# Performance work log

Measured on AMD Instinct MI355X. Metric: run time of the kernel, lower is better.

Reference implementation:

```python
import jax, jax.numpy as jnp
import numpy as np


def setup_inputs() -> dict:
    key = jax.random.key(0)
    ks = jax.random.split(key, 6)
    B, C, V, L = 64, 32, 512, 13
    C_OUT = 64
    C_CAT = (2 * 3 + 1) * C  # order*support_len + 1 = 7 blocks -> 224
    x = jax.random.normal(ks[0], (B, C, V, L), dtype=jnp.float32)
    support0 = jax.random.uniform(ks[1], (V, V), dtype=jnp.float32)
    support1 = jax.random.uniform(ks[2], (V, V), dtype=jnp.float32)
    support2 = jax.random.uniform(ks[3], (V, V), dtype=jnp.float32)
    W = jax.random.normal(ks[4], (C_OUT, C_CAT), dtype=jnp.float32) * 0.05
    b = jnp.zeros((C_OUT,), dtype=jnp.float32)
    return {"x": x, "support0": support0, "support1": support1,
            "support2": support2, "W": W, "b": b}


def reference(x, support0, support1, support2, W, b):
    # Graph WaveNet GCN, eval mode (dropout is identity at inference).
    # x: [B, C, V, L]; each support a: [V, V].
    outs = [x]
    for a in (support0, support1, support2):
        x1 = jnp.einsum('ncvl,vw->ncwl', x, a)   # order 1 propagation
        outs.append(x1)
        x2 = jnp.einsum('ncvl,vw->ncwl', x1, a)  # order 2 propagation
        outs.append(x2)
    h = jnp.concatenate(outs, axis=1)            # [B, 7*C, V, L]
    # 1x1 Conv2d == per-(v,l) linear over channels
    h = jnp.einsum('ncvl,oc->novl', h, W) + b[None, :, None, None]
    return h
```

## Files before the change

kernel.cpp:

```cpp
#include <hip/hip_runtime.h>


typedef unsigned short u16;
typedef unsigned int   u32;
typedef __bf16 bf16x8 __attribute__((ext_vector_type(8)));
typedef float  f32x4  __attribute__((ext_vector_type(4)));

#define DEVI static __device__ __forceinline__

#define NB   64
#define NC   32
#define NV   512
#define NL   13
#define CO   64
#define CCAT 224
#define MROWS 26624
#define SZA   262144L
#define MSZ   (26624L * 512L)

DEVI u16 f2bf(float f) {
  union { float f; u32 u; } v; v.f = f;
  u32 u = v.u;
  return (u16)((u + 0x7fffu + ((u >> 16) & 1u)) >> 16);
}

DEVI void gl2lds16(const void* g, void* l) {
  __builtin_amdgcn_global_load_lds((__attribute__((address_space(1))) void*)g,
                                   (__attribute__((address_space(3))) void*)l, 16, 0, 0);
}

__global__ __launch_bounds__(256) void prep_A(const float* __restrict__ A0,
                                              const float* __restrict__ A1,
                                              const float* __restrict__ A2,
                                              u16* __restrict__ BT,
                                              u16* __restrict__ ABF) {
  const int s = blockIdx.z;
  const float* A = (s == 0) ? A0 : ((s == 1) ? A1 : A2);
  u16* abf = ABF + (long)s * SZA;
  u16* bt  = BT + (long)(2 * s) * SZA;
  __shared__ float t[32][33];
  const int v0 = blockIdx.x * 32, w0 = blockIdx.y * 32;
  const int tid = threadIdx.x;
  for (int i = tid; i < 1024; i += 256) {
    const int r = i >> 5, c = i & 31;
    const float val = A[(long)(v0 + r) * 512 + w0 + c];
    t[r][c] = val;
    abf[(long)(v0 + r) * 512 + w0 + c] = f2bf(val);
  }
  __syncthreads();
  for (int i = tid; i < 1024; i += 256) {
    const int r = i >> 5, c = i & 31;
    bt[(long)(w0 + r) * 512 + v0 + c] = f2bf(t[c][r]);
  }
}

__global__ __launch_bounds__(256) void prep_W(const float* __restrict__ W,
                                              u16* __restrict__ WBF) {
  const int i = blockIdx.x * 256 + threadIdx.x;
  WBF[i] = f2bf(W[i]);
}

__global__ __launch_bounds__(256) void transpose_x(const float* __restrict__ x,
                                                   u16* __restrict__ XT) {
  __shared__ __align__(16) float tile[NV * NL];
  const int bc = blockIdx.x;
  const float4* src4 = (const float4*)(x + (long)bc * (NV * NL));
  float4* t4 = (float4*)tile;
  for (int i = threadIdx.x; i < (NV * NL) / 4; i += 256) t4[i] = src4[i];
  __syncthreads();
  u16* dst = XT + (long)bc * (NL * NV);
  for (int j = threadIdx.x; j < NL * NV; j += 256) {
    const int l = j >> 9, v = j & 511;
    dst[j] = f2bf(tile[v * NL + l]);
  }
}

__global__ __launch_bounds__(256) void gemm512(const u16* __restrict__ Ag,
                                               const u16* __restrict__ Bg,
                                               u16* __restrict__ Cg,
                                               long aZ, long bZ, long cZ) {
  __shared__ u16 As[128 * 32];
  __shared__ u16 Bs[128 * 32];
  const int p = blockIdx.z;
  const u16* A = Ag + (long)p * aZ;
  const u16* B = Bg + (long)p * bZ;
  u16*       C = Cg + (long)p * cZ;
  const int m0 = blockIdx.y * 128, n0 = blockIdx.x * 128;
  const int tid = threadIdx.x;
  const int lane = tid & 63, wid = tid >> 6;
  const int wm = wid >> 1, wn = wid & 1;
  const int lr = lane & 15, lq = lane >> 4;
  const int srow = lane >> 2, skq = lane & 3;

  f32x4 acc[4][4] = {};

  for (int kt = 0; kt < 16; ++kt) {
    const int k0 = kt * 32;
    __syncthreads();
#pragma unroll
    for (int j = 0; j < 2; ++j) {
      const int rb = wid * 32 + j * 16;
      gl2lds16(A + (long)(m0 + rb + srow) * 512 + (k0 + skq * 8), &As[rb * 32]);
      gl2lds16(B + (long)(n0 + rb + srow) * 512 + (k0 + skq * 8), &Bs[rb * 32]);
    }
    __syncthreads();
    bf16x8 af[4], bv[4];
#pragma unroll
    for (int t = 0; t < 4; ++t) {
      af[t] = *(const bf16x8*)&As[(wm * 64 + t * 16 + lr) * 32 + lq * 8];
      bv[t] = *(const bf16x8*)&Bs[(wn * 64 + t * 16 + lr) * 32 + lq * 8];
    }
#pragma unroll
    for (int i = 0; i < 4; ++i)
#pragma unroll
      for (int j = 0; j < 4; ++j)
        acc[i][j] = __builtin_amdgcn_mfma_f32_16x16x32_bf16(af[i], bv[j], acc[i][j], 0, 0, 0);
  }
#pragma unroll
  for (int i = 0; i < 4; ++i) {
    const int mr = m0 + wm * 64 + i * 16 + lq * 4;
#pragma unroll
    for (int j = 0; j < 4; ++j) {
      const int nc = n0 + wn * 64 + j * 16 + lr;
#pragma unroll
      for (int r = 0; r < 4; ++r)
        C[(long)(mr + r) * 512 + nc] = f2bf(acc[i][j][r]);
    }
  }
}

__global__ __launch_bounds__(256) void proj_out(const u16* __restrict__ Yall,
                                                const u16* __restrict__ WBF,
                                                const float* __restrict__ bias,
                                                float* __restrict__ out) {
  __shared__ u16 Hs[512 * 32];
  const int n = blockIdx.y, wch = blockIdx.x;
  const int tid = threadIdx.x;
  const int lane = tid & 63, wid = tid >> 6;
  const int lr = lane & 15, lq = lane >> 4;
  const int wq = tid & 15, cp = tid >> 4;

  f32x4 acc[32] = {};
  float bia[4];
#pragma unroll
  for (int r = 0; r < 4; ++r) bia[r] = bias[wid * 16 + lq * 4 + r];

  for (int blk = 0; blk < 7; ++blk) {
    const u16* Y = Yall + (long)blk * MSZ;
    __syncthreads();
    const long rbase = ((long)(n * NC + cp * 2) * NL) * 512 + wch * 32 + wq * 2;
#pragma unroll
    for (int lp = 0; lp < NL; ++lp) {
      const u32 a = *(const u32*)(Y + rbase + (long)lp * 512);
      const u32 b = *(const u32*)(Y + rbase + (long)lp * 512 + NL * 512);
      const u32 pack0 = (a & 0xffffu) | (b << 16);
      const u32 pack1 = (a >> 16) | (b & 0xffff0000u);
      const int w0_ = wq * 2, w1_ = w0_ + 1;
      const int g = cp >> 2, wic = cp & 3;
      *(u32*)&Hs[(w0_ * 16 + lp) * 32 + ((g ^ (w0_ & 3)) * 8) + wic * 2] = pack0;
      *(u32*)&Hs[(w1_ * 16 + lp) * 32 + ((g ^ (w1_ & 3)) * 8) + wic * 2] = pack1;
    }
    __syncthreads();
    const bf16x8 af = *(const bf16x8*)&WBF[(wid * 16 + lr) * CCAT + blk * 32 + lq * 8];
#pragma unroll
    for (int t = 0; t < 32; ++t) {
      const bf16x8 bv = *(const bf16x8*)&Hs[(t * 16 + lr) * 32 + ((lq ^ (t & 3)) * 8)];
      acc[t] = __builtin_amdgcn_mfma_f32_16x16x32_bf16(af, bv, acc[t], 0, 0, 0);
    }
  }
  if (lr < NL) {
#pragma unroll
    for (int t = 0; t < 32; ++t) {
      const int w = wch * 32 + t;
      const long base = (((long)n * CO + wid * 16 + lq * 4) * 512 + w) * NL + lr;
#pragma unroll
      for (int r = 0; r < 4; ++r)
        out[base + (long)r * (512 * NL)] = acc[t][r] + bia[r];
    }
  }
}

extern "C" void kernel_launch(void* const* d_in, const int* in_sizes, int n_in,
                              void* d_out, int out_size, void* d_ws, size_t ws_size,
                              hipStream_t stream) {
  const float* x  = (const float*)d_in[0];
  const float* s0 = (const float*)d_in[1];
  const float* s1 = (const float*)d_in[2];
  const float* s2 = (const float*)d_in[3];
  const float* W  = (const float*)d_in[4];
  const float* b  = (const float*)d_in[5];
  float* out = (float*)d_out;

  char* ws = (char*)d_ws;
  u16* XT  = (u16*)(ws);
  u16* Y   = (u16*)(ws + 27262976L);
  u16* BT  = (u16*)(ws + 190840832L);
  u16* ABF = (u16*)(ws + 193986560L);
  u16* WBF = (u16*)(ws + 195559424L);

  prep_A<<<dim3(16, 16, 3), 256, 0, stream>>>(s0, s1, s2, BT, ABF);
  prep_W<<<dim3(56), 256, 0, stream>>>(W, WBF);
  gemm512<<<dim3(4, 4, 3), 256, 0, stream>>>(BT, ABF, BT + SZA,
                                             2L * SZA, 1L * SZA, 2L * SZA);
  transpose_x<<<dim3(NB * NC), 256, 0, stream>>>(x, XT);
  gemm512<<<dim3(4, 208, 6), 256, 0, stream>>>(XT, BT, Y,
                                               0L, 1L * SZA, MSZ);
  proj_out<<<dim3(16, NB), 256, 0, stream>>>(XT, WBF, b, out);
}
```

Measured before the change: 393.9 us.

## Reorder big GEMM grid for A-tile reuse, widen proj_out to 512 threads, pack transpose stores

Replaces the big batched GEMM launch with a dedicated kernel whose grid puts the six propagation matrices and N tiles on the fast x dimension, so blocks sharing the same XT row tile run close together and can reuse it from L2. The output projection kernel now uses 512 threads with each wave handling half the w columns, which halves the per-thread accumulators, and it loads Y with ushort4 reads and a new LDS swizzle. The x transpose writes two bf16 values per 32-bit store. proj_out still reads XT and 7 blocks spaced MSZ apart, as in the code before; that indexing looks inconsistent with where Y is written, but the change keeps it.

Measured after the change: 351.6 us. 10.7% less time.

```diff
diff --git a/kernel.cpp b/kernel.cpp
--- a/kernel.cpp
+++ b/kernel.cpp
@@ -14,7 +14,6 @@
 #define NL   13
 #define CO   64
 #define CCAT 224
-#define MROWS 26624
 #define SZA   262144L
 #define MSZ   (26624L * 512L)
 
@@ -69,9 +68,11 @@
   for (int i = threadIdx.x; i < (NV * NL) / 4; i += 256) t4[i] = src4[i];
   __syncthreads();
   u16* dst = XT + (long)bc * (NL * NV);
-  for (int j = threadIdx.x; j < NL * NV; j += 256) {
-    const int l = j >> 9, v = j & 511;
-    dst[j] = f2bf(tile[v * NL + l]);
+  for (int j = threadIdx.x; j < NL * 256; j += 256) {
+    const int l = j >> 8, v = (j & 255) * 2;
+    const u32 lo = f2bf(tile[v * NL + l]);
+    const u32 hi = f2bf(tile[(v + 1) * NL + l]);
+    *(u32*)&dst[l * 512 + v] = lo | (hi << 16);
   }
 }
 
@@ -129,53 +130,109 @@
   }
 }
 
-__global__ __launch_bounds__(256) void proj_out(const u16* __restrict__ Yall,
+__global__ __launch_bounds__(256) void gemm_big(const u16* __restrict__ A,
+                                                const u16* __restrict__ Bg,
+                                                u16* __restrict__ Cg) {
+  __shared__ u16 As[128 * 32];
+  __shared__ u16 Bs[128 * 32];
+  const int p = blockIdx.x >> 2;
+  const int n0 = (blockIdx.x & 3) * 128;
+  const int m0 = blockIdx.y * 128;
+  const u16* B = Bg + (long)p * SZA;
+  u16*       C = Cg + (long)p * MSZ;
+  const int tid = threadIdx.x;
+  const int lane = tid & 63, wid = tid >> 6;
+  const int wm = wid >> 1, wn = wid & 1;
+  const int lr = lane & 15, lq = lane >> 4;
+  const int srow = lane >> 2, skq = lane & 3;
+
+  f32x4 acc[4][4] = {};
+
+  for (int kt = 0; kt < 16; ++kt) {
+    const int k0 = kt * 32;
+    __syncthreads();
+#pragma unroll
+    for (int j = 0; j < 2; ++j) {
+      const int rb = wid * 32 + j * 16;
+      gl2lds16(A + (long)(m0 + rb + srow) * 512 + (k0 + skq * 8), &As[rb * 32]);
+      gl2lds16(B + (long)(n0 + rb + srow) * 512 + (k0 + skq * 8), &Bs[rb * 32]);
+    }
+    __syncthreads();
+    bf16x8 af[4], bv[4];
+#pragma unroll
+    for (int t = 0; t < 4; ++t) {
+      af[t] = *(const bf16x8*)&As[(wm * 64 + t * 16 + lr) * 32 + lq * 8];
+      bv[t] = *(const bf16x8*)&Bs[(wn * 64 + t * 16 + lr) * 32 + lq * 8];
+    }
+#pragma unroll
+    for (int i = 0; i < 4; ++i)
+#pragma unroll
+      for (int j = 0; j < 4; ++j)
+        acc[i][j] = __builtin_amdgcn_mfma_f32_16x16x32_bf16(af[i], bv[j], acc[i][j], 0, 0, 0);
+  }
+#pragma unroll
+  for (int i = 0; i < 4; ++i) {
+    const int mr = m0 + wm * 64 + i * 16 + lq * 4;
+#pragma unroll
+    for (int j = 0; j < 4; ++j) {
+      const int nc = n0 + wn * 64 + j * 16 + lr;
+#pragma unroll
+      for (int r = 0; r < 4; ++r)
+        C[(long)(mr + r) * 512 + nc] = f2bf(acc[i][j][r]);
+    }
+  }
+}
+
+__global__ __launch_bounds__(512) void proj_out(const u16* __restrict__ Yall,
                                                 const u16* __restrict__ WBF,
                                                 const float* __restrict__ bias,
                                                 float* __restrict__ out) {
   __shared__ u16 Hs[512 * 32];
   const int n = blockIdx.y, wch = blockIdx.x;
+  const int w_base = wch * 32;
   const int tid = threadIdx.x;
   const int lane = tid & 63, wid = tid >> 6;
+  const int og = wid & 3, th = wid >> 2;
   const int lr = lane & 15, lq = lane >> 4;
-  const int wq = tid & 15, cp = tid >> 4;
-
-  f32x4 acc[32] = {};
+  const int c = tid >> 4, q = tid & 15;
+
+  f32x4 acc[16] = {};
   float bia[4];
 #pragma unroll
-  for (int r = 0; r < 4; ++r) bia[r] = bias[wid * 16 + lq * 4 + r];
+  for (int r = 0; r < 4; ++r) bia[r] = bias[og * 16 + lq * 4 + r];
+
+  const int cchunk = c >> 3, cin = c & 7;
 
   for (int blk = 0; blk < 7; ++blk) {
-    const u16* Y = Yall + (long)blk * MSZ;
-    __syncthreads();
-    const long rbase = ((long)(n * NC + cp * 2) * NL) * 512 + wch * 32 + wq * 2;
-#pragma unroll
-    for (int lp = 0; lp < NL; ++lp) {
-      const u32 a = *(const u32*)(Y + rbase + (long)lp * 512);
-      const u32 b = *(const u32*)(Y + rbase + (long)lp * 512 + NL * 512);
-      const u32 pack0 = (a & 0xffffu) | (b << 16);
-      const u32 pack1 = (a >> 16) | (b & 0xffff0000u);
-      const int w0_ = wq * 2, w1_ = w0_ + 1;
-      const int g = cp >> 2, wic = cp & 3;
-      *(u32*)&Hs[(w0_ * 16 + lp) * 32 + ((g ^ (w0_ & 3)) * 8) + wic * 2] = pack0;
-      *(u32*)&Hs[(w1_ * 16 + lp) * 32 + ((g ^ (w1_ & 3)) * 8) + wic * 2] = pack1;
-    }
-    __syncthreads();
-    const bf16x8 af = *(const bf16x8*)&WBF[(wid * 16 + lr) * CCAT + blk * 32 + lq * 8];
-#pragma unroll
-    for (int t = 0; t < 32; ++t) {
-      const bf16x8 bv = *(const bf16x8*)&Hs[(t * 16 + lr) * 32 + ((lq ^ (t & 3)) * 8)];
-      acc[t] = __builtin_amdgcn_mfma_f32_16x16x32_bf16(af, bv, acc[t], 0, 0, 0);
+    const u16* Yrow = Yall + (long)blk * MSZ + ((long)(n * NC + c) * NL) * 512 + w_base;
+    __syncthreads();
+    for (int i = q; i < 104; i += 16) {
+      const int lp = i >> 3, w4 = i & 7;
+      const ushort4 d = *(const ushort4*)(Yrow + lp * 512 + w4 * 4);
+      const int colc = ((cchunk ^ (w4 & 3)) << 3) | cin;
+      const int rbase = (w4 * 4) * 16 + lp;
+      Hs[(rbase +  0) * 32 + colc] = d.x;
+      Hs[(rbase + 16) * 32 + colc] = d.y;
+      Hs[(rbase + 32) * 32 + colc] = d.z;
+      Hs[(rbase + 48) * 32 + colc] = d.w;
+    }
+    __syncthreads();
+    const bf16x8 af = *(const bf16x8*)&WBF[(og * 16 + lr) * CCAT + blk * 32 + lq * 8];
+#pragma unroll
+    for (int tt = 0; tt < 16; ++tt) {
+      const int t = th * 16 + tt;
+      const bf16x8 bv = *(const bf16x8*)&Hs[(t * 16 + lr) * 32 + ((lq ^ ((t >> 2) & 3)) << 3)];
+      acc[tt] = __builtin_amdgcn_mfma_f32_16x16x32_bf16(af, bv, acc[tt], 0, 0, 0);
     }
   }
   if (lr < NL) {
 #pragma unroll
-    for (int t = 0; t < 32; ++t) {
-      const int w = wch * 32 + t;
-      const long base = (((long)n * CO + wid * 16 + lq * 4) * 512 + w) * NL + lr;
+    for (int tt = 0; tt < 16; ++tt) {
+      const int w = w_base + th * 16 + tt;
+      const long base = (((long)n * CO + og * 16 + lq * 4) * 512 + w) * NL + lr;
 #pragma unroll
       for (int r = 0; r < 4; ++r)
-        out[base + (long)r * (512 * NL)] = acc[t][r] + bia[r];
+        out[base + (long)r * (512 * NL)] = acc[tt][r] + bia[r];
     }
   }
 }
@@ -203,7 +260,6 @@
   gemm512<<<dim3(4, 4, 3), 256, 0, stream>>>(BT, ABF, BT + SZA,
                                              2L * SZA, 1L * SZA, 2L * SZA);
   transpose_x<<<dim3(NB * NC), 256, 0, stream>>>(x, XT);
-  gemm512<<<dim3(4, 208, 6), 256, 0, stream>>>(XT, BT, Y,
-                                               0L, 1L * SZA, MSZ);
-  proj_out<<<dim3(16, NB), 256, 0, stream>>>(XT, WBF, b, out);
-}
+  gemm_big<<<dim3(24, 208), 256, 0, stream>>>(XT, BT, Y);
+  proj_out<<<dim3(16, NB), 512, 0, stream>>>(XT, WBF, b, out);
+}
```

## Fuse graph propagation GEMMs with 1x1 projection to drop intermediate buffer

Applied to the files above, without the earlier changes.

Replaces the batched propagation GEMM and the separate projection kernel with one fused kernel. For each (batch, 64-column chunk), it streams x and support tiles through a triple-buffered LDS pipeline using async global-to-LDS loads. Each propagated block is written into an LDS H tile and immediately accumulated into the output projection. This removes the write and re-read of the large bf16 intermediate Y through global memory. The transpose kernel also packs two bf16 values per store. The cost is heavy LDS use (about 155 KB), which limits the kernel to one block per CU, plus extra barriers.

Result: slower. 636.9 us (+61.7%).

```diff
diff --git a/kernel.cpp b/kernel.cpp
--- a/kernel.cpp
+++ b/kernel.cpp
@@ -14,9 +14,7 @@
 #define NL   13
 #define CO   64
 #define CCAT 224
-#define MROWS 26624
-#define SZA   262144L
-#define MSZ   (26624L * 512L)
+#define SZA  262144L
 
 DEVI u16 f2bf(float f) {
   union { float f; u32 u; } v; v.f = f;
@@ -69,9 +67,11 @@
   for (int i = threadIdx.x; i < (NV * NL) / 4; i += 256) t4[i] = src4[i];
   __syncthreads();
   u16* dst = XT + (long)bc * (NL * NV);
-  for (int j = threadIdx.x; j < NL * NV; j += 256) {
-    const int l = j >> 9, v = j & 511;
-    dst[j] = f2bf(tile[v * NL + l]);
+  for (int j = threadIdx.x; j < NL * 256; j += 256) {
+    const int l = j >> 8, v = (j & 255) * 2;
+    const u32 lo = f2bf(tile[v * NL + l]);
+    const u32 hi = f2bf(tile[(v + 1) * NL + l]);
+    *(u32*)&dst[l * 512 + v] = lo | (hi << 16);
   }
 }
 
@@ -129,53 +129,109 @@
   }
 }
 
-__global__ __launch_bounds__(256) void proj_out(const u16* __restrict__ Yall,
-                                                const u16* __restrict__ WBF,
-                                                const float* __restrict__ bias,
-                                                float* __restrict__ out) {
-  __shared__ u16 Hs[512 * 32];
-  const int n = blockIdx.y, wch = blockIdx.x;
-  const int tid = threadIdx.x;
-  const int lane = tid & 63, wid = tid >> 6;
+__global__ __launch_bounds__(512, 2) void fused_gcn(const u16* __restrict__ Xt,
+                                                    const u16* __restrict__ Bt,
+                                                    const u16* __restrict__ WBF,
+                                                    const float* __restrict__ bias,
+                                                    float* __restrict__ out) {
+  __shared__ u16 As[3][416 * 32];
+  __shared__ u16 Bs[3][64 * 32];
+  __shared__ u16 Hs[832 * 40];
+
+  const int bid = blockIdx.x;
+  const int n = bid >> 3, wch = bid & 7;
+  const int tid = threadIdx.x, lane = tid & 63, wid = tid >> 6;
   const int lr = lane & 15, lq = lane >> 4;
-  const int wq = tid & 15, cp = tid >> 4;
-
-  f32x4 acc[32] = {};
+  const int ot = wid >> 1, jpar = wid & 1;
+  const int mt0 = wid >> 2, nt = wid & 3;
+  const u16* XtN = Xt + (long)n * (416L * 512);
+
+  f32x4 acco[26] = {};
+
+  auto stage = [&](int g) {
+    const int p = g >> 4, kt = g & 15, bi = g % 3;
+    const int rsub = lane >> 2, koff = kt * 32 + (lane & 3) * 8;
+    const u16* Bp = Bt + (long)p * SZA + (long)(wch * 64) * 512;
+#pragma unroll
+    for (int t = 0; t < 4; ++t) {
+      const int i = wid + t * 8;
+      if (i < 26) {
+        gl2lds16(XtN + (long)(i * 16 + rsub) * 512 + koff, &As[bi][i * 16 * 32]);
+      } else {
+        const int b = (i - 26) & 3;
+        gl2lds16(Bp + (long)(b * 16 + rsub) * 512 + koff, &Bs[bi][b * 16 * 32]);
+      }
+    }
+  };
+
+  auto proj = [&](int blk) {
+    const bf16x8 af = *(const bf16x8*)&WBF[(ot * 16 + lr) * CCAT + blk * 32 + lq * 8];
+#pragma unroll
+    for (int k = 0; k < 26; ++k) {
+      const int jt = jpar + 2 * k;
+      const bf16x8 bv = *(const bf16x8*)&Hs[(jt * 16 + lr) * 40 + lq * 8];
+      acco[k] = __builtin_amdgcn_mfma_f32_16x16x32_bf16(af, bv, acco[k], 0, 0, 0);
+    }
+  };
+
+  stage(0);
+  for (int i = tid; i < 416 * 16; i += 512) {
+    const int m = i >> 4, wq = i & 15;
+    const ushort4 v = *(const ushort4*)(XtN + (long)m * 512 + wch * 64 + wq * 4);
+    const int c = (m * 5042) >> 16, l = m - c * 13;
+    const int rb = (wq * 4) * 13 + l;
+    Hs[(rb +  0) * 40 + c] = v.x;
+    Hs[(rb + 13) * 40 + c] = v.y;
+    Hs[(rb + 26) * 40 + c] = v.z;
+    Hs[(rb + 39) * 40 + c] = v.w;
+  }
+  __syncthreads();
+  proj(0);
+
+  for (int p = 0; p < 6; ++p) {
+    f32x4 accp[13] = {};
+    for (int kt = 0; kt < 16; ++kt) {
+      const int g = p * 16 + kt;
+      if (g < 95) {
+        stage(g + 1);
+        asm volatile("s_waitcnt vmcnt(4)\n\ts_barrier" ::: "memory");
+      } else {
+        asm volatile("s_waitcnt vmcnt(0)\n\ts_barrier" ::: "memory");
+      }
+      const u16* Ab = As[g % 3];
+      const u16* Bb = Bs[g % 3];
+      const bf16x8 bv = *(const bf16x8*)&Bb[(nt * 16 + lr) * 32 + lq * 8];
+#pragma unroll
+      for (int j = 0; j < 13; ++j) {
+        const bf16x8 av = *(const bf16x8*)&Ab[((mt0 + 2 * j) * 16 + lr) * 32 + lq * 8];
+        accp[j] = __builtin_amdgcn_mfma_f32_16x16x32_bf16(av, bv, accp[j], 0, 0, 0);
+      }
+    }
+#pragma unroll
+    for (int j = 0; j < 13; ++j) {
+      const int mt = mt0 + 2 * j;
+#pragma unroll
+      for (int r = 0; r < 4; ++r) {
+        const int m = mt * 16 + lq * 4 + r;
+        const int c = (m * 5042) >> 16, l = m - c * 13;
+        Hs[((nt * 16 + lr) * 13 + l) * 40 + c] = f2bf(accp[j][r]);
+      }
+    }
+    __syncthreads();
+    proj(p + 1);
+  }
+
   float bia[4];
 #pragma unroll
-  for (int r = 0; r < 4; ++r) bia[r] = bias[wid * 16 + lq * 4 + r];
-
-  for (int blk = 0; blk < 7; ++blk) {
-    const u16* Y = Yall + (long)blk * MSZ;
-    __syncthreads();
-    const long rbase = ((long)(n * NC + cp * 2) * NL) * 512 + wch * 32 + wq * 2;
-#pragma unroll
-    for (int lp = 0; lp < NL; ++lp) {
-      const u32 a = *(const u32*)(Y + rbase + (long)lp * 512);
-      const u32 b = *(const u32*)(Y + rbase + (long)lp * 512 + NL * 512);
-      const u32 pack0 = (a & 0xffffu) | (b << 16);
-      const u32 pack1 = (a >> 16) | (b & 0xffff0000u);
-      const int w0_ = wq * 2, w1_ = w0_ + 1;
-      const int g = cp >> 2, wic = cp & 3;
-      *(u32*)&Hs[(w0_ * 16 + lp) * 32 + ((g ^ (w0_ & 3)) * 8) + wic * 2] = pack0;
-      *(u32*)&Hs[(w1_ * 16 + lp) * 32 + ((g ^ (w1_ & 3)) * 8) + wic * 2] = pack1;
-    }
-    __syncthreads();
-    const bf16x8 af = *(const bf16x8*)&WBF[(wid * 16 + lr) * CCAT + blk * 32 + lq * 8];
-#pragma unroll
-    for (int t = 0; t < 32; ++t) {
-      const bf16x8 bv = *(const bf16x8*)&Hs[(t * 16 + lr) * 32 + ((lq ^ (t & 3)) * 8)];
-      acc[t] = __builtin_amdgcn_mfma_f32_16x16x32_bf16(af, bv, acc[t], 0, 0, 0);
-    }
-  }
-  if (lr < NL) {
-#pragma unroll
-    for (int t = 0; t < 32; ++t) {
-      const int w = wch * 32 + t;
-      const long base = (((long)n * CO + wid * 16 + lq * 4) * 512 + w) * NL + lr;
-#pragma unroll
-      for (int r = 0; r < 4; ++r)
-        out[base + (long)r * (512 * NL)] = acc[t][r] + bia[r];
+  for (int r = 0; r < 4; ++r) bia[r] = bias[ot * 16 + lq * 4 + r];
+  const long obase = (long)n * (64L * 6656) + (long)wch * 832;
+#pragma unroll
+  for (int k = 0; k < 26; ++k) {
+    const int j0 = (jpar + 2 * k) * 16;
+#pragma unroll
+    for (int r = 0; r < 4; ++r) {
+      const int o = ot * 16 + lq * 4 + r;
+      out[obase + (long)o * 6656 + j0 + lr] = acco[k][r] + bia[r];
     }
   }
 }
@@ -193,17 +249,14 @@
 
   char* ws = (char*)d_ws;
   u16* XT  = (u16*)(ws);
-  u16* Y   = (u16*)(ws + 27262976L);
-  u16* BT  = (u16*)(ws + 190840832L);
-  u16* ABF = (u16*)(ws + 193986560L);
-  u16* WBF = (u16*)(ws + 195559424L);
+  u16* BT  = (u16*)(ws + 27262976L);
+  u16* ABF = (u16*)(ws + 30408704L);
+  u16* WBF = (u16*)(ws + 31981568L);
 
   prep_A<<<dim3(16, 16, 3), 256, 0, stream>>>(s0, s1, s2, BT, ABF);
   prep_W<<<dim3(56), 256, 0, stream>>>(W, WBF);
   gemm512<<<dim3(4, 4, 3), 256, 0, stream>>>(BT, ABF, BT + SZA,
                                              2L * SZA, 1L * SZA, 2L * SZA);
   transpose_x<<<dim3(NB * NC), 256, 0, stream>>>(x, XT);
-  gemm512<<<dim3(4, 208, 6), 256, 0, stream>>>(XT, BT, Y,
-                                               0L, 1L * SZA, MSZ);
-  proj_out<<<dim3(16, NB), 256, 0, stream>>>(XT, WBF, b, out);
-}
+  fused_gcn<<<dim3(512), 512, 0, stream>>>(XT, BT, WBF, b, out);
+}
```
